# Kernel optimization log

Hardware: AMD Instinct MI355X
Metric: run time of the kernel (lower is better)

## Reference

```python
import jax, jax.numpy as jnp
import numpy as np

KS = 7
HEADS = 8


def _conv1x1(a, w, b):
    # a: (B,Cin,H,W), w: (Cout,Cin), b: (Cout,)
    return jnp.einsum('bchw,oc->bohw', a, w) + b[None, :, None, None]


def _unfold2d(a, ks):
    # a: (B,C,Hp,Wp) -> (B,C,H,W,ks,ks) sliding windows, stride 1
    H = a.shape[2] - ks + 1
    W = a.shape[3] - ks + 1
    ii = jnp.arange(H)[:, None] + jnp.arange(ks)[None, :]  # (H,ks)
    jj = jnp.arange(W)[:, None] + jnp.arange(ks)[None, :]  # (W,ks)
    return a[:, :, ii[:, None, :, None], jj[None, :, None, :]]


def setup_inputs() -> dict:
    key = jax.random.key(0)
    ks = jax.random.split(key, 10)
    B, C, H, W = 4, 128, 56, 56
    x = jax.random.normal(ks[0], (B, C, H, W), dtype=jnp.float32)
    sc = 1.0 / np.sqrt(C)
    q_w = jax.random.normal(ks[1], (C, C), dtype=jnp.float32) * sc
    q_b = jax.random.normal(ks[2], (C,), dtype=jnp.float32) * 0.01
    k_w = jax.random.normal(ks[3], (C, C), dtype=jnp.float32) * sc
    k_b = jax.random.normal(ks[4], (C,), dtype=jnp.float32) * 0.01
    v_w = jax.random.normal(ks[5], (C, C), dtype=jnp.float32) * sc
    v_b = jax.random.normal(ks[6], (C,), dtype=jnp.float32) * 0.01
    rel_h = jax.random.normal(ks[7], (C // 2, KS, 1), dtype=jnp.float32)
    rel_w = jax.random.normal(ks[8], (C // 2, 1, KS), dtype=jnp.float32)
    return {'x': x, 'q_w': q_w, 'q_b': q_b, 'k_w': k_w, 'k_b': k_b,
            'v_w': v_w, 'v_b': v_b, 'rel_h': rel_h, 'rel_w': rel_w}


def reference(x, q_w, q_b, k_w, k_b, v_w, v_b, rel_h, rel_w):
    B, C, H, W = x.shape
    dkh = C // HEADS
    K2 = KS * KS
    pl = (KS - 1) // 2
    pr = KS - 1 - pl
    xp = jnp.pad(x, ((0, 0), (0, 0), (pl, pr), (pl, pr)))

    k = _conv1x1(xp, k_w, k_b)
    v = _conv1x1(xp, v_w, v_b)
    q = _conv1x1(x, q_w, q_b)

    # unfold K/V into (B,C,H,W,KS,KS) then reshape exactly as torch does
    # (this reshape intermixes channel/window axes; replicated faithfully)
    k6 = _unfold2d(k, KS).reshape(B, HEADS, H, W, dkh, K2)
    v6 = _unfold2d(v, KS).reshape(B, HEADS, H, W, dkh, K2)
    q6 = q.reshape(B, HEADS, H, W, dkh, 1)

    # q^T k over the dkh axis -> (B,heads,H,W,KS,KS)
    qk = jnp.einsum('bhxyd,bhxydk->bhxyk', q6[..., 0], k6)
    qk = qk.reshape(B, HEADS, H, W, KS, KS)

    # einsum 'bhxydz,cij->bhxyij' has no shared index: factorizes as
    # (sum over d,z of q) * (sum over c of rel)
    qsum = q6.sum(axis=(4, 5))  # (B,heads,H,W)
    qk = qk + qsum[..., None, None] * rel_h.sum(axis=0)  # (KS,1) broadcast
    qk = qk + qsum[..., None, None] * rel_w.sum(axis=0)  # (1,KS) broadcast

    w = jax.nn.softmax(qk.reshape(B, HEADS, H, W, K2), axis=-1)
    out = jnp.einsum('bhxyk,bhxydk->bhxyd', w, v6)  # (B,heads,H,W,dvh)
    return out.reshape(B, C, H, W)
```

## Files before the change

### kernel.cpp

```cpp
#include <hip/hip_runtime.h>
#include <hip/hip_bf16.h>
#include <math.h>

#define NB    4
#define NC    128
#define NPIX  3136
#define NPPIX 3844
#define CHW   401408
#define CPHW  492032
#define KPAD_N 1968128
#define SKS   68

template <int CTRL, int RM>
__device__ __forceinline__ float dpp_mov(float x, float old) {
    return __int_as_float(__builtin_amdgcn_update_dpp(
        __float_as_int(old), __float_as_int(x), CTRL, RM, 0xf, false));
}
__device__ __forceinline__ float wave_max(float x) {
    x = fmaxf(x, dpp_mov<0x111, 0xf>(x, x));
    x = fmaxf(x, dpp_mov<0x112, 0xf>(x, x));
    x = fmaxf(x, dpp_mov<0x114, 0xf>(x, x));
    x = fmaxf(x, dpp_mov<0x118, 0xf>(x, x));
    x = fmaxf(x, dpp_mov<0x142, 0xa>(x, x));
    x = fmaxf(x, dpp_mov<0x143, 0xc>(x, x));
    return __int_as_float(__builtin_amdgcn_readlane(__float_as_int(x), 63));
}
__device__ __forceinline__ float wave_sum(float x) {
    x = x + dpp_mov<0x111, 0xf>(x, 0.f);
    x = x + dpp_mov<0x112, 0xf>(x, 0.f);
    x = x + dpp_mov<0x114, 0xf>(x, 0.f);
    x = x + dpp_mov<0x118, 0xf>(x, 0.f);
    x = x + dpp_mov<0x142, 0xa>(x, 0.f);
    x = x + dpp_mov<0x143, 0xc>(x, 0.f);
    return __int_as_float(__builtin_amdgcn_readlane(__float_as_int(x), 63));
}

__global__ __launch_bounds__(256) void prep_kernel(
    const float* __restrict__ qw, const float* __restrict__ kw,
    const float* __restrict__ vw,
    const float* __restrict__ kb, const float* __restrict__ vb,
    const float* __restrict__ rel_h, const float* __restrict__ rel_w,
    float* __restrict__ kpad, float* __restrict__ vpad,
    float* __restrict__ w4q, float* __restrict__ w4k, float* __restrict__ w4v,
    float* __restrict__ rb)
{
    int idx = blockIdx.x * 256 + threadIdx.x;
    {
        int img = idx / 708;
        int hl = idx - img * 708;
        int p;
        if (hl < 186) p = hl;
        else if (hl < 372) p = 3658 + (hl - 186);
        else {
            int j = hl - 372;
            int r = j / 6, cc = j - r * 6;
            p = (r + 3) * 62 + (cc < 3 ? cc : cc + 56);
        }
        int ch = img & 127;
        size_t o = (size_t)img * NPPIX + p;
        kpad[o] = kb[ch];
        vpad[o] = vb[ch];
    }
    if (idx < 3 * 16384) {
        int m = idx >> 14;
        int r = idx & 16383;
        int cc = r & 3;
        int t = r >> 2;
        int o = t & 127;
        int c4 = t >> 7;
        const float* src = (m == 0) ? qw : (m == 1) ? kw : vw;
        float* dst = (m == 0) ? w4q : (m == 1) ? w4k : w4v;
        dst[r] = src[o * 128 + c4 * 4 + cc];
    }
    if (idx < 14) {
        const float* src = (idx < 7) ? rel_h : rel_w;
        int off = (idx < 7) ? idx : idx - 7;
        float s = 0.f;
        for (int c = 0; c < 64; ++c) s += src[c * 7 + off];
        rb[idx] = s;
    }
}

__global__ __launch_bounds__(256) void conv_kernel(
    const float* __restrict__ x,
    const float* __restrict__ w4q, const float* __restrict__ w4k,
    const float* __restrict__ w4v,
    const float* __restrict__ qb, const float* __restrict__ kb,
    const float* __restrict__ vb,
    float* __restrict__ q, float* __restrict__ kpad, float* __restrict__ vpad)
{
    __shared__ float sx[128 * 16];
    __shared__ float st[128 * 18];
    int bid = blockIdx.x;
    int tile = bid % 196;
    int b = bid / 196;
    int pix0 = tile * 16;
    const float* xb = x + b * CHW + pix0;

    for (int i = threadIdx.x; i < 512; i += 256) {
        int c = i >> 2, p4 = (i & 3) * 4;
        *(float4*)(sx + c * 16 + p4) = *(const float4*)(xb + c * NPIX + p4);
    }
    __syncthreads();

    int lane = threadIdx.x & 63;
    int wave = threadIdx.x >> 6;
    int o = wave * 32 + (lane & 31);
    int ph = (lane >> 5) * 8;
    const float4* Wq = (const float4*)w4q + o;
    const float4* Wk = (const float4*)w4k + o;
    const float4* Wv = (const float4*)w4v + o;

    float aq[8] = {}, ak[8] = {}, av[8] = {};
    #pragma unroll 2
    for (int c4 = 0; c4 < 32; ++c4) {
        float4 wq4 = Wq[c4 * 128];
        float4 wk4 = Wk[c4 * 128];
        float4 wv4 = Wv[c4 * 128];
        float wqr[4] = {wq4.x, wq4.y, wq4.z, wq4.w};
        float wkr[4] = {wk4.x, wk4.y, wk4.z, wk4.w};
        float wvr[4] = {wv4.x, wv4.y, wv4.z, wv4.w};
        #pragma unroll
        for (int cc = 0; cc < 4; ++cc) {
            const float* xr = sx + (c4 * 4 + cc) * 16 + ph;
            float4 xa = *(const float4*)xr;
            float4 xc = *(const float4*)(xr + 4);
            float xv[8] = {xa.x, xa.y, xa.z, xa.w, xc.x, xc.y, xc.z, xc.w};
            #pragma unroll
            for (int p = 0; p < 8; ++p) {
                aq[p] += wqr[cc] * xv[p];
                ak[p] += wkr[cc] * xv[p];
                av[p] += wvr[cc] * xv[p];
            }
        }
    }
    float bq = qb[o], bk = kb[o], bv = vb[o];

    int pix = threadIdx.x & 15;
    int o8 = (threadIdx.x >> 4) * 8;
    int pp = pix0 + pix;
    int yy = pp / 56, xx = pp - yy * 56;
    int po = (yy + 3) * 62 + xx + 3;
    float* wr = st + o * 18 + ph;

    {
        #pragma unroll
        for (int p = 0; p < 8; ++p) wr[p] = aq[p] + bq;
        __syncthreads();
        float* qd = q + b * CHW + pix0 + pix;
        #pragma unroll
        for (int i = 0; i < 8; ++i)
            qd[(o8 + i) * NPIX] = st[(o8 + i) * 18 + pix];
    }
    {
        __syncthreads();
        #pragma unroll
        for (int p = 0; p < 8; ++p) wr[p] = ak[p] + bk;
        __syncthreads();
        float* kd = kpad + (size_t)b * CPHW + po;
        #pragma unroll
        for (int i = 0; i < 8; ++i)
            kd[(size_t)(o8 + i) * NPPIX] = st[(o8 + i) * 18 + pix];
    }
    {
        __syncthreads();
        #pragma unroll
        for (int p = 0; p < 8; ++p) wr[p] = av[p] + bv;
        __syncthreads();
        float* vd = vpad + (size_t)b * CPHW + po;
        #pragma unroll
        for (int i = 0; i < 8; ++i)
            vd[(size_t)(o8 + i) * NPPIX] = st[(o8 + i) * 18 + pix];
    }
}

__global__ __launch_bounds__(256) void attn_kernel(
    const float* __restrict__ q, const float* __restrict__ kpad,
    const float* __restrict__ vpad, const float* __restrict__ rb,
    float* __restrict__ out)
{
    __shared__ float sK[20 * SKS];
    __shared__ float sV[21 * SKS];
    __shared__ float sW[4 * 64];
    int bid = blockIdx.x;
    int qpart = bid & 3;
    int bc = bid >> 2;
    const float* qc = q + bc * NPIX + 784 * qpart;
    const float* kc = kpad + (size_t)bc * NPPIX + (14 * qpart) * 62;
    const float* vc = vpad + (size_t)bc * NPPIX + (14 * qpart) * 62;
    float* oc = out + bc * NPIX + 784 * qpart;

    for (int i = threadIdx.x; i < 20 * 62; i += 256) {
        int yy = i / 62, xx = i - yy * 62;
        sK[yy * SKS + xx] = kc[i];
        sV[yy * SKS + xx] = vc[i];
    }
    for (int i = threadIdx.x; i < SKS; i += 256) sV[20 * SKS + i] = 0.f;
    __syncthreads();

    int lane = threadIdx.x & 63;
    int wave = threadIdx.x >> 6;
    int k2 = min(lane, 48);
    int di = k2 / 7, dj = k2 - di * 7;
    float rbias = rb[di] + rb[7 + dj];
    int koff = di * SKS + dj;
    int t16 = lane & 15, p = lane >> 4;
    float* sWw = sW + wave * 64;

    for (int gl = wave; gl < 49; gl += 4) {
        int ul0 = gl * 16;
        int y0 = ul0 / 56;
        int x0 = ul0 - y0 * 56;

        int ulu = __builtin_amdgcn_readfirstlane(ul0);
        float4 q0 = *(const float4*)(qc + ulu);
        float4 q1 = *(const float4*)(qc + ulu + 4);
        float4 q2 = *(const float4*)(qc + ulu + 8);
        float4 q3 = *(const float4*)(qc + ulu + 12);
        float qa[16] = {q0.x, q0.y, q0.z, q0.w, q1.x, q1.y, q1.z, q1.w,
                        q2.x, q2.y, q2.z, q2.w, q3.x, q3.y, q3.z, q3.w};
        float qs = 0.f;
        #pragma unroll
        for (int t = 0; t < 16; ++t) qs += qa[t];

        float acc = 0.f;
        const float* kb_ = sK + y0 * SKS + x0 + koff;
        if (x0 != 48) {
            #pragma unroll
            for (int t = 0; t < 16; ++t) acc += qa[t] * kb_[t];
        } else {
            const float* kb2 = sK + (y0 + 1) * SKS + koff;
            #pragma unroll
            for (int t = 0; t < 8; ++t) acc += qa[t] * kb_[t];
            #pragma unroll
            for (int t = 0; t < 8; ++t) acc += qa[8 + t] * kb2[t];
        }
        float val = (lane < 49) ? (acc + qs * rbias) : -1e30f;

        float mS = wave_max(val);
        float e = __expf(val - mS);
        float sS = wave_sum(e);
        float wgt = e * __builtin_amdgcn_rcpf(sS);
        sWw[lane] = wgt;

        int u = ul0 + t16;
        int yt = u / 56;
        int xt = u - yt * 56;
        const float* vbase = sV + yt * SKS + xt + p * (2 * SKS);
        const float* wbase = sWw + p * 14;
        float oacc = 0.f;
        #pragma unroll
        for (int j = 0; j < 7; ++j) oacc += wbase[j] * vbase[j];
        #pragma unroll
        for (int j = 0; j < 7; ++j) oacc += wbase[7 + j] * vbase[SKS + j];
        oacc += __shfl_xor(oacc, 16);
        oacc += __shfl_xor(oacc, 32);
        if (lane < 16) oc[ul0 + lane] = oacc;
    }
}

extern "C" void kernel_launch(void* const* d_in, const int* in_sizes, int n_in,
                              void* d_out, int out_size, void* d_ws, size_t ws_size,
                              hipStream_t stream) {
    const float* x     = (const float*)d_in[0];
    const float* qw    = (const float*)d_in[1];
    const float* qb    = (const float*)d_in[2];
    const float* kw    = (const float*)d_in[3];
    const float* kb    = (const float*)d_in[4];
    const float* vw    = (const float*)d_in[5];
    const float* vb    = (const float*)d_in[6];
    const float* rel_h = (const float*)d_in[7];
    const float* rel_w = (const float*)d_in[8];
    float* out = (float*)d_out;

    float* ws   = (float*)d_ws;
    float* kpad = ws;
    float* vpad = kpad + KPAD_N;
    float* qbuf = vpad + KPAD_N;
    float* w4q  = qbuf + 1605632;
    float* w4k  = w4q + 16384;
    float* w4v  = w4k + 16384;
    float* rb   = w4v + 16384;

    prep_kernel<<<1416, 256, 0, stream>>>(qw, kw, vw, kb, vb, rel_h, rel_w,
                                          kpad, vpad, w4q, w4k, w4v, rb);
    conv_kernel<<<784, 256, 0, stream>>>(x, w4q, w4k, w4v, qb, kb, vb,
                                         qbuf, kpad, vpad);
    attn_kernel<<<2048, 256, 0, stream>>>(qbuf, kpad, vpad, rb, out);
}
```

Baseline: 72.60 us.

## Drop padded K/V buffers, synthesize border bias in attention, prefetch weights and q

K and V are now stored unpadded. The attention kernel fills the halo with the bias value when it loads tiles into shared memory, so the prep kernel no longer writes border bias and launches far fewer blocks. The conv kernel stages q, k and v in one shared buffer with a single barrier, uses a new stride, and software-prefetches the next weight float4s. The attention kernel also prefetches the next q group. This trades extra bounds checks in the tile load for less global memory traffic and fewer barriers.

```diff
diff --git a/kernel.cpp b/kernel.cpp
--- a/kernel.cpp
+++ b/kernel.cpp
@@ -5,11 +5,9 @@
 #define NB    4
 #define NC    128
 #define NPIX  3136
-#define NPPIX 3844
 #define CHW   401408
-#define CPHW  492032
-#define KPAD_N 1968128
 #define SKS   68
+#define STS   19
 
 template <int CTRL, int RM>
 __device__ __forceinline__ float dpp_mov(float x, float old) {
@@ -38,29 +36,11 @@
 __global__ __launch_bounds__(256) void prep_kernel(
     const float* __restrict__ qw, const float* __restrict__ kw,
     const float* __restrict__ vw,
-    const float* __restrict__ kb, const float* __restrict__ vb,
     const float* __restrict__ rel_h, const float* __restrict__ rel_w,
-    float* __restrict__ kpad, float* __restrict__ vpad,
     float* __restrict__ w4q, float* __restrict__ w4k, float* __restrict__ w4v,
     float* __restrict__ rb)
 {
     int idx = blockIdx.x * 256 + threadIdx.x;
-    {
-        int img = idx / 708;
-        int hl = idx - img * 708;
-        int p;
-        if (hl < 186) p = hl;
-        else if (hl < 372) p = 3658 + (hl - 186);
-        else {
-            int j = hl - 372;
-            int r = j / 6, cc = j - r * 6;
-            p = (r + 3) * 62 + (cc < 3 ? cc : cc + 56);
-        }
-        int ch = img & 127;
-        size_t o = (size_t)img * NPPIX + p;
-        kpad[o] = kb[ch];
-        vpad[o] = vb[ch];
-    }
     if (idx < 3 * 16384) {
         int m = idx >> 14;
         int r = idx & 16383;
@@ -87,10 +67,10 @@
     const float* __restrict__ w4v,
     const float* __restrict__ qb, const float* __restrict__ kb,
     const float* __restrict__ vb,
-    float* __restrict__ q, float* __restrict__ kpad, float* __restrict__ vpad)
+    float* __restrict__ q, float* __restrict__ kbuf, float* __restrict__ vbuf)
 {
     __shared__ float sx[128 * 16];
-    __shared__ float st[128 * 18];
+    __shared__ float st[3 * 128 * STS];
     int bid = blockIdx.x;
     int tile = bid % 196;
     int b = bid / 196;
@@ -111,20 +91,28 @@
     const float4* Wk = (const float4*)w4k + o;
     const float4* Wv = (const float4*)w4v + o;
 
+    float4 wqc = Wq[0], wkc = Wk[0], wvc = Wv[0];
     float aq[8] = {}, ak[8] = {}, av[8] = {};
-    #pragma unroll 2
+    #pragma unroll 1
     for (int c4 = 0; c4 < 32; ++c4) {
-        float4 wq4 = Wq[c4 * 128];
-        float4 wk4 = Wk[c4 * 128];
-        float4 wv4 = Wv[c4 * 128];
+        float4 xs[8];
+        #pragma unroll
+        for (int cc = 0; cc < 4; ++cc) {
+            xs[2 * cc]     = *(const float4*)(sx + (c4 * 4 + cc) * 16 + ph);
+            xs[2 * cc + 1] = *(const float4*)(sx + (c4 * 4 + cc) * 16 + ph + 4);
+        }
+        float4 wq4 = wqc, wk4 = wkc, wv4 = wvc;
+        if (c4 < 31) {
+            wqc = Wq[(c4 + 1) * 128];
+            wkc = Wk[(c4 + 1) * 128];
+            wvc = Wv[(c4 + 1) * 128];
+        }
         float wqr[4] = {wq4.x, wq4.y, wq4.z, wq4.w};
         float wkr[4] = {wk4.x, wk4.y, wk4.z, wk4.w};
         float wvr[4] = {wv4.x, wv4.y, wv4.z, wv4.w};
         #pragma unroll
         for (int cc = 0; cc < 4; ++cc) {
-            const float* xr = sx + (c4 * 4 + cc) * 16 + ph;
-            float4 xa = *(const float4*)xr;
-            float4 xc = *(const float4*)(xr + 4);
+            float4 xa = xs[2 * cc], xc = xs[2 * cc + 1];
             float xv[8] = {xa.x, xa.y, xa.z, xa.w, xc.x, xc.y, xc.z, xc.w};
             #pragma unroll
             for (int p = 0; p < 8; ++p) {
@@ -135,49 +123,36 @@
         }
     }
     float bq = qb[o], bk = kb[o], bv = vb[o];
+    float* wrq = st + o * STS + ph;
+    float* wrk = st + 128 * STS + o * STS + ph;
+    float* wrv = st + 2 * 128 * STS + o * STS + ph;
+    #pragma unroll
+    for (int p = 0; p < 8; ++p) {
+        wrq[p] = aq[p] + bq;
+        wrk[p] = ak[p] + bk;
+        wrv[p] = av[p] + bv;
+    }
+    __syncthreads();
 
     int pix = threadIdx.x & 15;
     int o8 = (threadIdx.x >> 4) * 8;
-    int pp = pix0 + pix;
-    int yy = pp / 56, xx = pp - yy * 56;
-    int po = (yy + 3) * 62 + xx + 3;
-    float* wr = st + o * 18 + ph;
-
-    {
-        #pragma unroll
-        for (int p = 0; p < 8; ++p) wr[p] = aq[p] + bq;
-        __syncthreads();
-        float* qd = q + b * CHW + pix0 + pix;
-        #pragma unroll
-        for (int i = 0; i < 8; ++i)
-            qd[(o8 + i) * NPIX] = st[(o8 + i) * 18 + pix];
-    }
-    {
-        __syncthreads();
-        #pragma unroll
-        for (int p = 0; p < 8; ++p) wr[p] = ak[p] + bk;
-        __syncthreads();
-        float* kd = kpad + (size_t)b * CPHW + po;
-        #pragma unroll
-        for (int i = 0; i < 8; ++i)
-            kd[(size_t)(o8 + i) * NPPIX] = st[(o8 + i) * 18 + pix];
-    }
-    {
-        __syncthreads();
-        #pragma unroll
-        for (int p = 0; p < 8; ++p) wr[p] = av[p] + bv;
-        __syncthreads();
-        float* vd = vpad + (size_t)b * CPHW + po;
-        #pragma unroll
-        for (int i = 0; i < 8; ++i)
-            vd[(size_t)(o8 + i) * NPPIX] = st[(o8 + i) * 18 + pix];
+    float* qd = q + b * CHW + pix0 + pix;
+    float* kd = kbuf + b * CHW + pix0 + pix;
+    float* vd = vbuf + b * CHW + pix0 + pix;
+    #pragma unroll
+    for (int i = 0; i < 8; ++i) {
+        int r = o8 + i;
+        qd[r * NPIX] = st[r * STS + pix];
+        kd[r * NPIX] = st[128 * STS + r * STS + pix];
+        vd[r * NPIX] = st[2 * 128 * STS + r * STS + pix];
     }
 }
 
 __global__ __launch_bounds__(256) void attn_kernel(
-    const float* __restrict__ q, const float* __restrict__ kpad,
-    const float* __restrict__ vpad, const float* __restrict__ rb,
-    float* __restrict__ out)
+    const float* __restrict__ q, const float* __restrict__ kbuf,
+    const float* __restrict__ vbuf,
+    const float* __restrict__ kb, const float* __restrict__ vb,
+    const float* __restrict__ rb, float* __restrict__ out)
 {
     __shared__ float sK[20 * SKS];
     __shared__ float sV[21 * SKS];
@@ -185,15 +160,24 @@
     int bid = blockIdx.x;
     int qpart = bid & 3;
     int bc = bid >> 2;
+    int ch = bc & 127;
     const float* qc = q + bc * NPIX + 784 * qpart;
-    const float* kc = kpad + (size_t)bc * NPPIX + (14 * qpart) * 62;
-    const float* vc = vpad + (size_t)bc * NPPIX + (14 * qpart) * 62;
+    const float* kc = kbuf + bc * NPIX;
+    const float* vc = vbuf + bc * NPIX;
     float* oc = out + bc * NPIX + 784 * qpart;
+    float kbias = kb[ch], vbias = vb[ch];
+    int qr0 = 14 * qpart;
 
     for (int i = threadIdx.x; i < 20 * 62; i += 256) {
         int yy = i / 62, xx = i - yy * 62;
-        sK[yy * SKS + xx] = kc[i];
-        sV[yy * SKS + xx] = vc[i];
+        int gy = qr0 + yy - 3;
+        int gx = xx - 3;
+        bool in = (gy >= 0) && (gy < 56) && (gx >= 0) && (gx < 56);
+        int off = in ? gy * 56 + gx : 0;
+        float kv = in ? kc[off] : kbias;
+        float vv = in ? vc[off] : vbias;
+        sK[yy * SKS + xx] = kv;
+        sV[yy * SKS + xx] = vv;
     }
     for (int i = threadIdx.x; i < SKS; i += 256) sV[20 * SKS + i] = 0.f;
     __syncthreads();
@@ -207,16 +191,25 @@
     int t16 = lane & 15, p = lane >> 4;
     float* sWw = sW + wave * 64;
 
+    int ulu = __builtin_amdgcn_readfirstlane(wave * 16);
+    float4 p0 = *(const float4*)(qc + ulu);
+    float4 p1 = *(const float4*)(qc + ulu + 4);
+    float4 p2 = *(const float4*)(qc + ulu + 8);
+    float4 p3 = *(const float4*)(qc + ulu + 12);
+
     for (int gl = wave; gl < 49; gl += 4) {
         int ul0 = gl * 16;
         int y0 = ul0 / 56;
         int x0 = ul0 - y0 * 56;
 
-        int ulu = __builtin_amdgcn_readfirstlane(ul0);
-        float4 q0 = *(const float4*)(qc + ulu);
-        float4 q1 = *(const float4*)(qc + ulu + 4);
-        float4 q2 = *(const float4*)(qc + ulu + 8);
-        float4 q3 = *(const float4*)(qc + ulu + 12);
+        float4 q0 = p0, q1 = p1, q2 = p2, q3 = p3;
+        if (gl + 4 < 49) {
+            int un = __builtin_amdgcn_readfirstlane((gl + 4) * 16);
+            p0 = *(const float4*)(qc + un);
+            p1 = *(const float4*)(qc + un + 4);
+            p2 = *(const float4*)(qc + un + 8);
+            p3 = *(const float4*)(qc + un + 12);
+        }
         float qa[16] = {q0.x, q0.y, q0.z, q0.w, q1.x, q1.y, q1.z, q1.w,
                         q2.x, q2.y, q2.z, q2.w, q3.x, q3.y, q3.z, q3.w};
         float qs = 0.f;
@@ -274,17 +267,17 @@
     float* out = (float*)d_out;
 
     float* ws   = (float*)d_ws;
-    float* kpad = ws;
-    float* vpad = kpad + KPAD_N;
-    float* qbuf = vpad + KPAD_N;
+    float* kbuf = ws;
+    float* vbuf = kbuf + 1605632;
+    float* qbuf = vbuf + 1605632;
     float* w4q  = qbuf + 1605632;
     float* w4k  = w4q + 16384;
     float* w4v  = w4k + 16384;
     float* rb   = w4v + 16384;
 
-    prep_kernel<<<1416, 256, 0, stream>>>(qw, kw, vw, kb, vb, rel_h, rel_w,
-                                          kpad, vpad, w4q, w4k, w4v, rb);
+    prep_kernel<<<192, 256, 0, stream>>>(qw, kw, vw, rel_h, rel_w,
+                                         w4q, w4k, w4v, rb);
     conv_kernel<<<784, 256, 0, stream>>>(x, w4q, w4k, w4v, qb, kb, vb,
-                                         qbuf, kpad, vpad);
-    attn_kernel<<<2048, 256, 0, stream>>>(qbuf, kpad, vpad, rb, out);
-}
+                                         qbuf, kbuf, vbuf);
+    attn_kernel<<<2048, 256, 0, stream>>>(qbuf, kbuf, vbuf, kb, vb, rb, out);
+}
```

New measurement: 72.24 us. Within noise of the previous version (-0.5%).
